# Performance work log

Measured on AMD Instinct MI355X. Metric: run time of the kernel, lower is better.

Reference implementation:

```python
import jax, jax.numpy as jnp
import numpy as np

N, E, D, C = 100000, 1600000, 64, 16


def setup_inputs() -> dict:
    key = jax.random.key(0)
    ks = jax.random.split(key, 9)
    s = 0.1  # weight init scale
    return {
        "x": jax.random.normal(ks[0], (N, D), jnp.float32),
        "edge_index": jax.random.randint(ks[1], (2, E), 0, N),
        "edge_attr": jax.random.uniform(ks[2], (E, 1), jnp.float32),
        # SplineConv 1: kernel_size=3, degree=1, dim=1
        "W1": jax.random.normal(ks[3], (3, D, D), jnp.float32) * s,
        "root1": jax.random.normal(ks[4], (D, D), jnp.float32) * s,
        "b1": jnp.zeros((D,), jnp.float32),
        # SplineConv 2: kernel_size=5
        "W2": jax.random.normal(ks[5], (5, D, D), jnp.float32) * s,
        "root2": jax.random.normal(ks[6], (D, D), jnp.float32) * s,
        "b2": jnp.zeros((D,), jnp.float32),
        # MLP head
        "Wm1": jax.random.normal(ks[7], (D, D), jnp.float32) * s,
        "bm1": jnp.zeros((D,), jnp.float32),
        "Wm2": jax.random.normal(ks[8], (D, C), jnp.float32) * s,
        "bm2": jnp.zeros((C,), jnp.float32),
    }


def spline_conv(x, edge_index, pseudo, W, root, bias, K):
    """PyG SplineConv: dim=1, degree=1, open spline, aggr='mean', root+bias.

    Degree-1 open B-spline in 1D: v = p*(K-1); each edge hits kernel slots
    floor(v) and floor(v)+1 with weights (1-frac) and frac. Because the
    message x_j @ W[k] is linear, we aggregate coeff*x_j per slot first
    (segment_sum over dst), then do K small GEMMs [N,D]x[D,D].
    """
    src, dst = edge_index[0], edge_index[1]
    n = x.shape[0]
    v = pseudo[:, 0] * (K - 1)                      # [E]
    frac = v - jnp.floor(v)
    i0 = jnp.clip(jnp.floor(v).astype(jnp.int32), 0, K - 1)
    i1 = jnp.clip(i0 + 1, 0, K - 1)
    xj = x[src]                                      # [E, D] gather
    deg = jax.ops.segment_sum(jnp.ones((dst.shape[0],), x.dtype), dst,
                              num_segments=n)        # in-degree for mean
    out = jnp.zeros((n, W.shape[2]), x.dtype)
    for k in range(K):                               # small fixed K (3 or 5)
        coeff = (1.0 - frac) * (i0 == k) + frac * (i1 == k)   # [E]
        agg = jax.ops.segment_sum(xj * coeff[:, None], dst, num_segments=n)
        out = out + agg @ W[k]
    out = out / jnp.maximum(deg, 1.0)[:, None]
    return out + x @ root + bias


def reference(x, edge_index, edge_attr, W1, root1, b1, W2, root2, b2,
              Wm1, bm1, Wm2, bm2):
    # eval mode: dropout is identity
    h = jax.nn.elu(spline_conv(x, edge_index, edge_attr, W1, root1, b1, 3))
    h = jax.nn.elu(spline_conv(h, edge_index, edge_attr, W2, root2, b2, 5))
    h = jax.nn.relu(h @ Wm1 + bm1)
    return jax.nn.relu(h @ Wm2 + bm2)
```

## Files before the change

kernel.cpp:

```cpp
#include <hip/hip_runtime.h>
#include <cstdint>
#include <cstddef>


#define D_FEAT 64
#define AS_STRIDE 40
#define NB_MAX 1024
#define PART_B 128

typedef _Float16 half8v __attribute__((ext_vector_type(8)));
typedef _Float16 half4v __attribute__((ext_vector_type(4)));
typedef float f32x4 __attribute__((ext_vector_type(4)));

__device__ __forceinline__ float elu_f(float x) {
    return x > 0.f ? x : expm1f(x);
}


__global__ __launch_bounds__(256) void prep_k(
    const float* __restrict__ x, const int* __restrict__ edst,
    const float* __restrict__ W1, const float* __restrict__ root1,
    const float* __restrict__ W2, const float* __restrict__ root2,
    const float* __restrict__ Wm1, const float* __restrict__ Wm2,
    _Float16* __restrict__ xh, unsigned int* __restrict__ counts,
    _Float16* __restrict__ Wt1, _Float16* __restrict__ Wt2,
    _Float16* __restrict__ Wm1t, _Float16* __restrict__ Wm2t,
    int E, int chunk, int NBUCKET, int total8, int cvtB)
{
    __shared__ unsigned int hist[NB_MAX];
    int b = blockIdx.x, t = threadIdx.x;
    if (b < cvtB) {
        int i = b * 256 + t;
        if (i < total8) {
            const float4* src = (const float4*)(x + (size_t)i * 8);
            float4 v0 = src[0], v1 = src[1];
            half8v hv = { (_Float16)v0.x, (_Float16)v0.y, (_Float16)v0.z, (_Float16)v0.w,
                          (_Float16)v1.x, (_Float16)v1.y, (_Float16)v1.z, (_Float16)v1.w };
            ((half8v*)xh)[i] = hv;
        }
        return;
    }
    if (b < cvtB + PART_B) {
        int bb = b - cvtB;
        for (int i = t; i < NBUCKET; i += 256) hist[i] = 0u;
        __syncthreads();
        int e0 = bb * chunk;
        int e1 = e0 + chunk; if (e1 > E) e1 = E;
        for (int e = e0 + t; e < e1; e += 256)
            atomicAdd(&hist[edst[e] >> 7], 1u);
        __syncthreads();
        for (int i = t; i < NBUCKET; i += 256)
            counts[(size_t)i * PART_B + bb] = hist[i];
        return;
    }
    int i = (b - cvtB - PART_B) * 256 + t;
    if (i < 64 * 256) {
        int n = i >> 8, k = i & 255;
        float v = (k < 192) ? W1[k * 64 + n] : root1[(k - 192) * 64 + n];
        Wt1[n * 256 + k] = (_Float16)v;
    } else if (i < 64 * 256 + 64 * 384) {
        int j = i - 64 * 256;
        int n = j / 384, k = j % 384;
        float v = (k < 320) ? W2[k * 64 + n] : root2[(k - 320) * 64 + n];
        Wt2[n * 384 + k] = (_Float16)v;
    } else if (i < 64 * 256 + 64 * 384 + 64 * 64) {
        int j = i - 64 * 256 - 64 * 384;
        int n = j >> 6, k = j & 63;
        Wm1t[n * 64 + k] = (_Float16)Wm1[k * 64 + n];
    } else if (i < 64 * 256 + 64 * 384 + 64 * 64 + 16 * 64) {
        int j = i - 64 * 256 - 64 * 384 - 64 * 64;
        int n = j >> 6, k = j & 63;
        Wm2t[n * 64 + k] = (_Float16)Wm2[k * 16 + n];
    }
}


__global__ __launch_bounds__(256) void psum_k(
    const unsigned int* __restrict__ data, unsigned int* __restrict__ partial, int L)
{
    __shared__ unsigned int wsum[4];
    int i = blockIdx.x * 256 + threadIdx.x;
    int lane = threadIdx.x & 63, wid = threadIdx.x >> 6;
    unsigned int v = (i < L) ? data[i] : 0u;
    #pragma unroll
    for (int off = 32; off; off >>= 1) v += __shfl_xor(v, off);
    if (lane == 0) wsum[wid] = v;
    __syncthreads();
    if (threadIdx.x == 0)
        partial[blockIdx.x] = wsum[0] + wsum[1] + wsum[2] + wsum[3];
}

__global__ __launch_bounds__(512) void pscan_k(
    unsigned int* __restrict__ partial, int nb)
{
    __shared__ unsigned int wsum[8];
    int t = threadIdx.x, lane = t & 63, wid = t >> 6;
    unsigned int v = (t < nb) ? partial[t] : 0u;
    unsigned int orig = v;
    #pragma unroll
    for (int off = 1; off < 64; off <<= 1) {
        unsigned int s = __shfl_up(v, off);
        if (lane >= off) v += s;
    }
    if (lane == 63) wsum[wid] = v;
    __syncthreads();
    unsigned int add = 0;
    for (int i = 0; i < wid; ++i) add += wsum[i];
    if (t < nb) partial[t] = v + add - orig;
}

__global__ __launch_bounds__(256) void pwrite_k(
    unsigned int* __restrict__ data, const unsigned int* __restrict__ partial, int L)
{
    __shared__ unsigned int wsum[4];
    int i = blockIdx.x * 256 + threadIdx.x;
    int lane = threadIdx.x & 63, wid = threadIdx.x >> 6;
    unsigned int v = (i < L) ? data[i] : 0u;
    unsigned int orig = v;
    #pragma unroll
    for (int off = 1; off < 64; off <<= 1) {
        unsigned int s = __shfl_up(v, off);
        if (lane >= off) v += s;
    }
    if (lane == 63) wsum[wid] = v;
    __syncthreads();
    unsigned int add = partial[blockIdx.x];
    for (int w = 0; w < wid; ++w) add += wsum[w];
    if (i < L) data[i] = add + v - orig;
}


__global__ __launch_bounds__(256) void place_k(
    const int* __restrict__ esrc, const int* __restrict__ edst,
    const float* __restrict__ attr, const unsigned int* __restrict__ off,
    int2* __restrict__ staging, int E, int chunk, int NBUCKET)
{
    __shared__ unsigned int cur[NB_MAX];
    int t = threadIdx.x;
    for (int b = t; b < NBUCKET; b += 256)
        cur[b] = off[(size_t)b * PART_B + blockIdx.x];
    __syncthreads();
    int e0 = blockIdx.x * chunk;
    int e1 = e0 + chunk; if (e1 > E) e1 = E;
    for (int e = e0 + t; e < e1; e += 256) {
        int d = edst[e];
        unsigned int pos = atomicAdd(&cur[d >> 7], 1u);
        staging[pos] = make_int2(esrc[e] | ((d & 127) << 17), __float_as_int(attr[e]));
    }
}


__global__ __launch_bounds__(256) void binsort_k(
    const int2* __restrict__ staging, const unsigned int* __restrict__ off,
    unsigned int* __restrict__ slotptr,
    int2* __restrict__ rec3, int2* __restrict__ rec5,
    int N, int E, int NBUCKET)
{
    __shared__ unsigned int nh[512];
    __shared__ unsigned int curb[512];
    __shared__ unsigned int wsum[4];
    __shared__ float fdeg[128];
    int bkt = blockIdx.x, t = threadIdx.x;
    int node0 = bkt << 7;
    unsigned int start = off[(size_t)bkt * PART_B];
    unsigned int end = (bkt + 1 < NBUCKET) ? off[(size_t)(bkt + 1) * PART_B]
                                           : (unsigned int)E;
    nh[t] = 0u; nh[t + 256] = 0u;
    __syncthreads();
    for (unsigned int i = start + t; i < end; i += 256) {
        int2 r = staging[i];
        float p = __int_as_float(r.y);
        int q = (int)(p * 4.0f); q = q > 3 ? 3 : q;
        atomicAdd(&nh[(((r.x >> 17) & 127) << 2) | q], 1u);
    }
    __syncthreads();
    int lane = t & 63, wid = t >> 6;
    unsigned int v0 = nh[2 * t], v1 = nh[2 * t + 1];
    unsigned int pair = v0 + v1, inc = pair;
    #pragma unroll
    for (int o = 1; o < 64; o <<= 1) {
        unsigned int s = __shfl_up(inc, o);
        if (lane >= o) inc += s;
    }
    if (lane == 63) wsum[wid] = inc;
    __syncthreads();
    unsigned int wo = 0;
    for (int i = 0; i < wid; ++i) wo += wsum[i];
    unsigned int excl = wo + inc - pair;
    unsigned int b0 = start + excl, b1 = b0 + v0;
    curb[2 * t] = b0; curb[2 * t + 1] = b1;
    int j0 = 2 * t, j1 = 2 * t + 1;
    if (node0 + (j0 >> 2) < N) slotptr[(size_t)node0 * 4 + j0] = b0;
    if (node0 + (j1 >> 2) < N) slotptr[(size_t)node0 * 4 + j1] = b1;
    if (bkt == NBUCKET - 1 && t == 0) slotptr[(size_t)N * 4] = (unsigned int)E;
    if (bkt == NBUCKET - 1 && t < 4) {
        rec3[E + t] = make_int2(0, 0);
        rec5[E + t] = make_int2(0, 0);
    }
    __syncthreads();
    if (t < 128) {
        unsigned int s0 = curb[t << 2];
        unsigned int s1 = (t == 127) ? end : curb[(t << 2) + 4];
        fdeg[t] = 1.0f / fmaxf((float)(s1 - s0), 1.0f);
    }
    __syncthreads();
    for (unsigned int i = start + t; i < end; i += 256) {
        int2 r = staging[i];
        float p = __int_as_float(r.y);
        int q = (int)(p * 4.0f); q = q > 3 ? 3 : q;
        int nodeLocal = (r.x >> 17) & 127;
        unsigned int pos = atomicAdd(&curb[(nodeLocal << 2) | q], 1u);
        float fd = fdeg[nodeLocal];
        float fr5 = p * 4.0f - (float)q;
        float w15 = fr5 * fd, w05 = fd - w15;
        int i03 = q >> 1;
        float fr3 = p * 2.0f - (float)i03;
        float w13 = fr3 * fd, w03 = fd - w13;
        int src = r.x & 0x1FFFF;
        union { _Float16 h[2]; int i; } p5, p3;
        p5.h[0] = (_Float16)w05; p5.h[1] = (_Float16)w15;
        p3.h[0] = (_Float16)w03; p3.h[1] = (_Float16)w13;
        rec5[pos] = make_int2(src, p5.i);
        rec3[pos] = make_int2(src, p3.i);
    }
}


template<int K>
__global__ __launch_bounds__(256) void gather_k(
    const _Float16* __restrict__ xin,
    const int2* __restrict__ rec,
    const unsigned int* __restrict__ slotptr,
    _Float16* __restrict__ agg, int N)
{
    int n = blockIdx.x * 4 + (threadIdx.x >> 6);
    int lane = threadIdx.x & 63;
    if (n >= N) return;
    int sub = lane >> 4;
    int col = (lane & 15) << 2;
    unsigned int sp[5];
    #pragma unroll
    for (int q = 0; q < 5; ++q) sp[q] = slotptr[(size_t)n * 4 + q];
    half4v acc[K];
    #pragma unroll
    for (int k = 0; k < K; ++k) acc[k] = (half4v){0, 0, 0, 0};

    #pragma unroll
    for (int ph = 0; ph < 2; ++ph) {
        const int qA = ph, qB = ph + 2;
        const int kA = (K == 5) ? qA : (qA >> 1);
        const int kB = (K == 5) ? qB : (qB >> 1);
        unsigned int iA = sp[qA], endA = sp[qA + 1];
        unsigned int iB = sp[qB], endB = sp[qB + 1];
        while (iA < endA || iB < endB) {
            unsigned int eA = iA + (unsigned int)sub;
            unsigned int eB = iB + (unsigned int)sub;
            int2 rA = rec[eA];
            int2 rB = rec[eB];
            int wAi = (eA < endA) ? rA.y : 0;
            int wBi = (eB < endB) ? rB.y : 0;
            half4v rowA = *(const half4v*)(xin + (size_t)(unsigned)rA.x * D_FEAT + col);
            half4v rowB = *(const half4v*)(xin + (size_t)(unsigned)rB.x * D_FEAT + col);
            union { int i; _Float16 h[2]; } uA, uB;
            uA.i = wAi; uB.i = wBi;
            half4v w0A = {uA.h[0], uA.h[0], uA.h[0], uA.h[0]};
            half4v w1A = {uA.h[1], uA.h[1], uA.h[1], uA.h[1]};
            half4v w0B = {uB.h[0], uB.h[0], uB.h[0], uB.h[0]};
            half4v w1B = {uB.h[1], uB.h[1], uB.h[1], uB.h[1]};
            acc[kA]     += rowA * w0A;
            acc[kA + 1] += rowA * w1A;
            acc[kB]     += rowB * w0B;
            acc[kB + 1] += rowB * w1B;
            iA += 4; iB += 4;
        }
    }

    #pragma unroll
    for (int k = 0; k < K; ++k) {
        union { half4v h; int2 i; } u, s;
        u.h = acc[k];
        s.i.x = __shfl_xor(u.i.x, 16);
        s.i.y = __shfl_xor(u.i.y, 16);
        u.h += s.h;
        s.i.x = __shfl_xor(u.i.x, 32);
        s.i.y = __shfl_xor(u.i.y, 32);
        u.h += s.h;
        if (sub == 0)
            *(half4v*)(agg + ((size_t)n * K + k) * D_FEAT + col) = u.h;
    }
}


template<int K, bool DO_MLP>
__global__ __launch_bounds__(256) void gemm_mfma(
    const _Float16* __restrict__ A,
    const _Float16* __restrict__ X,
    const _Float16* __restrict__ Wt,
    const float* __restrict__ bias,
    const _Float16* __restrict__ Wm1t,
    const float* __restrict__ bm1,
    const _Float16* __restrict__ Wm2t,
    const float* __restrict__ bm2,
    _Float16* __restrict__ outh,
    float* __restrict__ outf,
    int N)
{
    constexpr int lenA = K * 64;
    constexpr int Kd = lenA + D_FEAT;
    constexpr int SMEM_H = DO_MLP ? (128 * 72 * 2) : (128 * AS_STRIDE + 64 * AS_STRIDE);
    __shared__ _Float16 smem[SMEM_H];
    _Float16* As = smem;
    _Float16* Bs = smem + 128 * AS_STRIDE;

    int t = threadIdx.x;
    int row0 = blockIdx.x * 128;
    int w = t >> 6, lane = t & 63;
    int m16 = lane & 15, q = lane >> 4;

    f32x4 acc[2][4];
    #pragma unroll
    for (int rf = 0; rf < 2; ++rf)
        #pragma unroll
        for (int c = 0; c < 4; ++c) acc[rf][c] = (f32x4){0.f, 0.f, 0.f, 0.f};

    int srow = t >> 1;
    int skh  = (t & 1) * 16;
    int bn   = t >> 2;
    int bkq  = (t & 3) * 8;

    int grow = row0 + srow; if (grow >= N) grow = N - 1;
    const _Float16* arowA = A + (size_t)grow * lenA;
    const _Float16* arowX = X + (size_t)grow * D_FEAT;

    for (int kk = 0; kk < Kd; kk += 32) {
        const _Float16* src = (kk < lenA) ? (arowA + kk + skh)
                                          : (arowX + (kk - lenA) + skh);
        half8v a0 = *(const half8v*)(src);
        half8v a1 = *(const half8v*)(src + 8);
        half8v b0 = *(const half8v*)(Wt + (size_t)bn * Kd + kk + bkq);
        __syncthreads();
        *(half8v*)(&As[srow * AS_STRIDE + skh]) = a0;
        *(half8v*)(&As[srow * AS_STRIDE + skh + 8]) = a1;
        *(half8v*)(&Bs[bn * AS_STRIDE + bkq]) = b0;
        __syncthreads();
        half8v af0 = *(const half8v*)(&As[(w * 32 + m16) * AS_STRIDE + q * 8]);
        half8v af1 = *(const half8v*)(&As[(w * 32 + 16 + m16) * AS_STRIDE + q * 8]);
        #pragma unroll
        for (int c = 0; c < 4; ++c) {
            half8v bf = *(const half8v*)(&Bs[(c * 16 + m16) * AS_STRIDE + q * 8]);
            acc[0][c] = __builtin_amdgcn_mfma_f32_16x16x32_f16(af0, bf, acc[0][c], 0, 0, 0);
            acc[1][c] = __builtin_amdgcn_mfma_f32_16x16x32_f16(af1, bf, acc[1][c], 0, 0, 0);
        }
    }

    if (!DO_MLP) {
        #pragma unroll
        for (int rf = 0; rf < 2; ++rf)
            #pragma unroll
            for (int c = 0; c < 4; ++c) {
                int colg = c * 16 + m16;
                float bb = bias[colg];
                #pragma unroll
                for (int r = 0; r < 4; ++r) {
                    int rowg = row0 + w * 32 + rf * 16 + q * 4 + r;
                    if (rowg < N)
                        outh[(size_t)rowg * D_FEAT + colg] = (_Float16)elu_f(acc[rf][c][r] + bb);
                }
            }
        return;
    }

    _Float16* Hs  = smem;
    _Float16* Hs2 = smem + 128 * 72;
    __syncthreads();
    #pragma unroll
    for (int rf = 0; rf < 2; ++rf)
        #pragma unroll
        for (int c = 0; c < 4; ++c) {
            int colg = c * 16 + m16;
            float bb = bias[colg];
            #pragma unroll
            for (int r = 0; r < 4; ++r)
                Hs[(w * 32 + rf * 16 + q * 4 + r) * 72 + colg] =
                    (_Float16)elu_f(acc[rf][c][r] + bb);
        }

    f32x4 acc3[2][4];
    #pragma unroll
    for (int rf = 0; rf < 2; ++rf)
        #pragma unroll
        for (int c = 0; c < 4; ++c) acc3[rf][c] = (f32x4){0.f, 0.f, 0.f, 0.f};
    #pragma unroll
    for (int kk = 0; kk < 64; kk += 32) {
        half8v af0 = *(const half8v*)(&Hs[(w * 32 + m16) * 72 + kk + q * 8]);
        half8v af1 = *(const half8v*)(&Hs[(w * 32 + 16 + m16) * 72 + kk + q * 8]);
        #pragma unroll
        for (int c = 0; c < 4; ++c) {
            half8v bf = *(const half8v*)(Wm1t + (size_t)(c * 16 + m16) * 64 + kk + q * 8);
            acc3[0][c] = __builtin_amdgcn_mfma_f32_16x16x32_f16(af0, bf, acc3[0][c], 0, 0, 0);
            acc3[1][c] = __builtin_amdgcn_mfma_f32_16x16x32_f16(af1, bf, acc3[1][c], 0, 0, 0);
        }
    }
    #pragma unroll
    for (int rf = 0; rf < 2; ++rf)
        #pragma unroll
        for (int c = 0; c < 4; ++c) {
            int colg = c * 16 + m16;
            float bb = bm1[colg];
            #pragma unroll
            for (int r = 0; r < 4; ++r)
                Hs2[(w * 32 + rf * 16 + q * 4 + r) * 72 + colg] =
                    (_Float16)fmaxf(acc3[rf][c][r] + bb, 0.f);
        }

    f32x4 acc4[2];
    acc4[0] = (f32x4){0.f, 0.f, 0.f, 0.f};
    acc4[1] = (f32x4){0.f, 0.f, 0.f, 0.f};
    #pragma unroll
    for (int kk = 0; kk < 64; kk += 32) {
        half8v af0 = *(const half8v*)(&Hs2[(w * 32 + m16) * 72 + kk + q * 8]);
        half8v af1 = *(const half8v*)(&Hs2[(w * 32 + 16 + m16) * 72 + kk + q * 8]);
        half8v bf = *(const half8v*)(Wm2t + (size_t)m16 * 64 + kk + q * 8);
        acc4[0] = __builtin_amdgcn_mfma_f32_16x16x32_f16(af0, bf, acc4[0], 0, 0, 0);
        acc4[1] = __builtin_amdgcn_mfma_f32_16x16x32_f16(af1, bf, acc4[1], 0, 0, 0);
    }
    float bb2 = bm2[m16];
    #pragma unroll
    for (int rf = 0; rf < 2; ++rf)
        #pragma unroll
        for (int r = 0; r < 4; ++r) {
            int rowg = row0 + w * 32 + rf * 16 + q * 4 + r;
            if (rowg < N)
                outf[(size_t)rowg * 16 + m16] = fmaxf(acc4[rf][r] + bb2, 0.f);
        }
}

extern "C" void kernel_launch(void* const* d_in, const int* in_sizes, int n_in,
                              void* d_out, int out_size, void* d_ws, size_t ws_size,
                              hipStream_t stream)
{
    const float* x     = (const float*)d_in[0];
    const int*   eidx  = (const int*)d_in[1];
    const float* attr  = (const float*)d_in[2];
    const float* W1    = (const float*)d_in[3];
    const float* root1 = (const float*)d_in[4];
    const float* b1    = (const float*)d_in[5];
    const float* W2    = (const float*)d_in[6];
    const float* root2 = (const float*)d_in[7];
    const float* b2    = (const float*)d_in[8];
    const float* Wm1   = (const float*)d_in[9];
    const float* bm1   = (const float*)d_in[10];
    const float* Wm2   = (const float*)d_in[11];
    const float* bm2   = (const float*)d_in[12];
    float* out = (float*)d_out;

    int N = in_sizes[0] / D_FEAT;
    int E = in_sizes[1] / 2;
    const int* esrc = eidx;
    const int* edst = eidx + E;
    int NBUCKET = (N + 127) >> 7;
    int chunk = (E + PART_B - 1) / PART_B;
    int L = NBUCKET * PART_B;
    int nbL = (L + 255) / 256;
    int total8 = N * D_FEAT / 8;
    int cvtB = (total8 + 255) / 256;
    int wElems = 64 * 256 + 64 * 384 + 64 * 64 + 16 * 64;
    int wB = (wElems + 255) / 256;

    _Float16* agg = (_Float16*)d_ws;
    _Float16* xh  = agg + (size_t)N * 5 * D_FEAT;
    _Float16* h   = xh + (size_t)N * D_FEAT;
    int2* staging = (int2*)(h + (size_t)N * D_FEAT);
    int2* rec3    = staging + E;
    int2* rec5    = rec3 + (E + 4);
    _Float16* Wt1 = (_Float16*)(rec5 + (E + 4));
    _Float16* Wt2 = Wt1 + 64 * 256;
    _Float16* Wm1t = Wt2 + 64 * 384;
    _Float16* Wm2t = Wm1t + 64 * 64;
    unsigned int* counts  = (unsigned int*)(Wm2t + 16 * 64);
    unsigned int* partial = counts + L;
    unsigned int* slotptr = partial + 512;

    dim3 blk(256);
    dim3 grid_w((N + 3) / 4);
    dim3 grid_g128((N + 127) / 128);

    prep_k<<<dim3(cvtB + PART_B + wB), blk, 0, stream>>>(
        x, edst, W1, root1, W2, root2, Wm1, Wm2,
        xh, counts, Wt1, Wt2, Wm1t, Wm2t, E, chunk, NBUCKET, total8, cvtB);

    psum_k<<<dim3(nbL), blk, 0, stream>>>(counts, partial, L);
    pscan_k<<<1, 512, 0, stream>>>(partial, nbL);
    pwrite_k<<<dim3(nbL), blk, 0, stream>>>(counts, partial, L);
    place_k<<<dim3(PART_B), blk, 0, stream>>>(esrc, edst, attr, counts, staging, E, chunk, NBUCKET);
    binsort_k<<<dim3(NBUCKET), blk, 0, stream>>>(staging, counts, slotptr, rec3, rec5, N, E, NBUCKET);

    gather_k<3><<<grid_w, blk, 0, stream>>>(xh, rec3, slotptr, agg, N);
    gemm_mfma<3, false><<<grid_g128, blk, 0, stream>>>(
        agg, xh, Wt1, b1, nullptr, nullptr, nullptr, nullptr, h, nullptr, N);

    gather_k<5><<<grid_w, blk, 0, stream>>>(h, rec5, slotptr, agg, N);
    gemm_mfma<5, true><<<grid_g128, blk, 0, stream>>>(
        agg, h, Wt2, b2, Wm1t, bm1, Wm2t, bm2, nullptr, out, N);
}
```

Baseline: 352.4 us.

## Share one edge record array across both spline convs and interleave four slot streams

Binsort now writes a single record array holding the source index plus fp16 (frac*invdeg, invdeg), and each gather kernel derives its K=3 or K=5 spline weights from those values in registers. This removes one E-sized int2 array write and its padding. The gather loop also walks all four quarter-slots together instead of two phases of two, issuing more independent loads per iteration to expose memory-level parallelism. The costs are extra fp16 arithmetic per edge, possible small precision differences from recomputing weights in half precision, and some wasted iterations when slot lengths differ.

After: 352.3 us. Within noise of the previous version (-0.0%).

```diff
diff --git a/kernel.cpp b/kernel.cpp
--- a/kernel.cpp
+++ b/kernel.cpp
@@ -152,8 +152,7 @@
 
 __global__ __launch_bounds__(256) void binsort_k(
     const int2* __restrict__ staging, const unsigned int* __restrict__ off,
-    unsigned int* __restrict__ slotptr,
-    int2* __restrict__ rec3, int2* __restrict__ rec5,
+    unsigned int* __restrict__ slotptr, int2* __restrict__ rec,
     int N, int E, int NBUCKET)
 {
     __shared__ unsigned int nh[512];
@@ -193,10 +192,6 @@
     if (node0 + (j0 >> 2) < N) slotptr[(size_t)node0 * 4 + j0] = b0;
     if (node0 + (j1 >> 2) < N) slotptr[(size_t)node0 * 4 + j1] = b1;
     if (bkt == NBUCKET - 1 && t == 0) slotptr[(size_t)N * 4] = (unsigned int)E;
-    if (bkt == NBUCKET - 1 && t < 4) {
-        rec3[E + t] = make_int2(0, 0);
-        rec5[E + t] = make_int2(0, 0);
-    }
     __syncthreads();
     if (t < 128) {
         unsigned int s0 = curb[t << 2];
@@ -212,16 +207,10 @@
         unsigned int pos = atomicAdd(&curb[(nodeLocal << 2) | q], 1u);
         float fd = fdeg[nodeLocal];
         float fr5 = p * 4.0f - (float)q;
-        float w15 = fr5 * fd, w05 = fd - w15;
-        int i03 = q >> 1;
-        float fr3 = p * 2.0f - (float)i03;
-        float w13 = fr3 * fd, w03 = fd - w13;
-        int src = r.x & 0x1FFFF;
-        union { _Float16 h[2]; int i; } p5, p3;
-        p5.h[0] = (_Float16)w05; p5.h[1] = (_Float16)w15;
-        p3.h[0] = (_Float16)w03; p3.h[1] = (_Float16)w13;
-        rec5[pos] = make_int2(src, p5.i);
-        rec3[pos] = make_int2(src, p3.i);
+        float w15 = fr5 * fd;
+        union { _Float16 h[2]; int i; } pr;
+        pr.h[0] = (_Float16)w15; pr.h[1] = (_Float16)fd;
+        rec[pos] = make_int2(r.x & 0x1FFFF, pr.i);
     }
 }
 
@@ -245,33 +234,42 @@
     #pragma unroll
     for (int k = 0; k < K; ++k) acc[k] = (half4v){0, 0, 0, 0};
 
-    #pragma unroll
-    for (int ph = 0; ph < 2; ++ph) {
-        const int qA = ph, qB = ph + 2;
-        const int kA = (K == 5) ? qA : (qA >> 1);
-        const int kB = (K == 5) ? qB : (qB >> 1);
-        unsigned int iA = sp[qA], endA = sp[qA + 1];
-        unsigned int iB = sp[qB], endB = sp[qB + 1];
-        while (iA < endA || iB < endB) {
-            unsigned int eA = iA + (unsigned int)sub;
-            unsigned int eB = iB + (unsigned int)sub;
-            int2 rA = rec[eA];
-            int2 rB = rec[eB];
-            int wAi = (eA < endA) ? rA.y : 0;
-            int wBi = (eB < endB) ? rB.y : 0;
-            half4v rowA = *(const half4v*)(xin + (size_t)(unsigned)rA.x * D_FEAT + col);
-            half4v rowB = *(const half4v*)(xin + (size_t)(unsigned)rB.x * D_FEAT + col);
-            union { int i; _Float16 h[2]; } uA, uB;
-            uA.i = wAi; uB.i = wBi;
-            half4v w0A = {uA.h[0], uA.h[0], uA.h[0], uA.h[0]};
-            half4v w1A = {uA.h[1], uA.h[1], uA.h[1], uA.h[1]};
-            half4v w0B = {uB.h[0], uB.h[0], uB.h[0], uB.h[0]};
-            half4v w1B = {uB.h[1], uB.h[1], uB.h[1], uB.h[1]};
-            acc[kA]     += rowA * w0A;
-            acc[kA + 1] += rowA * w1A;
-            acc[kB]     += rowB * w0B;
-            acc[kB + 1] += rowB * w1B;
-            iA += 4; iB += 4;
+    unsigned int it[4], en[4];
+    #pragma unroll
+    for (int q = 0; q < 4; ++q) { it[q] = sp[q] + (unsigned int)sub; en[q] = sp[q + 1]; }
+
+    while (it[0] < en[0] || it[1] < en[1] || it[2] < en[2] || it[3] < en[3]) {
+        bool v[4];
+        int2 r[4];
+        #pragma unroll
+        for (int q = 0; q < 4; ++q) {
+            v[q] = it[q] < en[q];
+            r[q] = rec[v[q] ? it[q] : 0u];
+        }
+        half4v row[4];
+        #pragma unroll
+        for (int q = 0; q < 4; ++q)
+            row[q] = *(const half4v*)(xin + (size_t)(unsigned)r[q].x * D_FEAT + col);
+        #pragma unroll
+        for (int q = 0; q < 4; ++q) {
+            int wi = v[q] ? r[q].y : 0;
+            union { int i; _Float16 h[2]; } u; u.i = wi;
+            _Float16 w15 = u.h[0], fd = u.h[1];
+            _Float16 w1, w0;
+            if (K == 5) {
+                w1 = w15;
+                w0 = (_Float16)(fd - w15);
+            } else {
+                const _Float16 hf = (_Float16)0.5f;
+                w1 = (q & 1) ? (_Float16)(hf * w15 + hf * fd) : (_Float16)(hf * w15);
+                w0 = (_Float16)(fd - w1);
+            }
+            const int k0 = (K == 5) ? q : (q >> 1);
+            half4v w0v = {w0, w0, w0, w0};
+            half4v w1v = {w1, w1, w1, w1};
+            acc[k0]     += row[q] * w0v;
+            acc[k0 + 1] += row[q] * w1v;
+            it[q] += 4;
         }
     }
 
@@ -471,9 +469,8 @@
     _Float16* xh  = agg + (size_t)N * 5 * D_FEAT;
     _Float16* h   = xh + (size_t)N * D_FEAT;
     int2* staging = (int2*)(h + (size_t)N * D_FEAT);
-    int2* rec3    = staging + E;
-    int2* rec5    = rec3 + (E + 4);
-    _Float16* Wt1 = (_Float16*)(rec5 + (E + 4));
+    int2* rec     = staging + E;
+    _Float16* Wt1 = (_Float16*)(rec + E);
     _Float16* Wt2 = Wt1 + 64 * 256;
     _Float16* Wm1t = Wt2 + 64 * 384;
     _Float16* Wm2t = Wm1t + 64 * 64;
@@ -493,13 +490,13 @@
     pscan_k<<<1, 512, 0, stream>>>(partial, nbL);
     pwrite_k<<<dim3(nbL), blk, 0, stream>>>(counts, partial, L);
     place_k<<<dim3(PART_B), blk, 0, stream>>>(esrc, edst, attr, counts, staging, E, chunk, NBUCKET);
-    binsort_k<<<dim3(NBUCKET), blk, 0, stream>>>(staging, counts, slotptr, rec3, rec5, N, E, NBUCKET);
-
-    gather_k<3><<<grid_w, blk, 0, stream>>>(xh, rec3, slotptr, agg, N);
+    binsort_k<<<dim3(NBUCKET), blk, 0, stream>>>(staging, counts, slotptr, rec, N, E, NBUCKET);
+
+    gather_k<3><<<grid_w, blk, 0, stream>>>(xh, rec, slotptr, agg, N);
     gemm_mfma<3, false><<<grid_g128, blk, 0, stream>>>(
         agg, xh, Wt1, b1, nullptr, nullptr, nullptr, nullptr, h, nullptr, N);
 
-    gather_k<5><<<grid_w, blk, 0, stream>>>(h, rec5, slotptr, agg, N);
+    gather_k<5><<<grid_w, blk, 0, stream>>>(h, rec, slotptr, agg, N);
     gemm_mfma<5, true><<<grid_g128, blk, 0, stream>>>(
         agg, h, Wt2, b2, Wm1t, bm1, Wm2t, bm2, nullptr, out, N);
 }
```
